# Optimization experiments

Measured on AMD Instinct MI355X. Metric: run time of the kernel, lower is better.

Reference implementation:

```python
import jax, jax.numpy as jnp
import numpy as np

B, S, D, H = 4, 1024, 1024, 16
DK = D // H
EPS = 1e-6

def setup_inputs() -> dict:
    key = jax.random.key(0)
    ks = jax.random.split(key, 7)
    scale = 1.0 / np.sqrt(D)
    return {
        "query": jax.random.normal(ks[0], (B, S, D), jnp.float32),
        "key": jax.random.normal(ks[1], (B, S, D), jnp.float32),
        "value": jax.random.normal(ks[2], (B, S, D), jnp.float32),
        "Wq": jax.random.normal(ks[3], (D, D), jnp.float32) * scale,
        "Wk": jax.random.normal(ks[4], (D, D), jnp.float32) * scale,
        "Wv": jax.random.normal(ks[5], (D, D), jnp.float32) * scale,
        "Wo": jax.random.normal(ks[6], (D, D), jnp.float32) * scale,
        "ln_gamma": jnp.ones((D,), jnp.float32),
        "ln_beta": jnp.zeros((D,), jnp.float32),
    }

def reference(query, key, value, Wq, Wk, Wv, Wo, ln_gamma, ln_beta):
    residual = query
    # projections (torch Linear: x @ W.T); reshape to [B,H,S,DK]
    def proj(x, W):
        y = jnp.einsum('bsd,ed->bse', x, W)
        return y.reshape(B, S, H, DK).transpose(0, 2, 1, 3)
    q, k, v = proj(query, Wq), proj(key, Wk), proj(value, Wv)
    scores = jnp.einsum('bhqd,bhkd->bhqk', q, k) / jnp.sqrt(jnp.float32(DK))
    p = jax.nn.softmax(scores, axis=-1)
    x = jnp.einsum('bhqk,bhkd->bhqd', p, v)
    x = x.transpose(0, 2, 1, 3).reshape(B, S, D)
    x = jnp.einsum('bsd,ed->bse', x, Wo)
    x = x + residual
    mu = jnp.mean(x, axis=-1, keepdims=True)
    var = jnp.var(x, axis=-1, keepdims=True)
    x = (x - mu) / jnp.sqrt(var + EPS) * ln_gamma + ln_beta
    return x
```

## Files before the change

kernel.cpp:

```cpp
#include <hip/hip_runtime.h>
#include <hip/hip_bf16.h>

#define B_ 4
#define S_ 1024
#define D_ 1024
#define H_ 16
#define DK_ 64
#define MROWS (B_*S_)

typedef short bf16x8 __attribute__((ext_vector_type(8)));
typedef float f32x4 __attribute__((ext_vector_type(4)));
typedef unsigned short u16;
typedef unsigned u32;
typedef u16 u16x4 __attribute__((ext_vector_type(4)));

__device__ __forceinline__ u16 f2bf(float f) {
    union { float f; unsigned u; } v; v.f = f;
    unsigned u = v.u;
    u += 0x7fff + ((u >> 16) & 1);
    return (u16)(u >> 16);
}

__device__ __forceinline__ void gld_lds16(const u16* gp, u16* lp) {
    __builtin_amdgcn_global_load_lds(
        (const __attribute__((address_space(1))) void*)gp,
        (__attribute__((address_space(3))) void*)lp,
        16, 0, 0);
}

__global__ __launch_bounds__(256) void pack_bf16(
    const float* __restrict__ q, const float* __restrict__ k, const float* __restrict__ v,
    const float* __restrict__ wq, const float* __restrict__ wk,
    const float* __restrict__ wv, const float* __restrict__ wo,
    u16* __restrict__ act_dst, u16* __restrict__ w_dst)
{
    const int NACT = 3 * MROWS * D_;
    const int NW   = 4 * D_ * D_;
    for (int c = blockIdx.x * blockDim.x + threadIdx.x;
         c < (NACT + NW) / 4; c += gridDim.x * blockDim.x) {
        int e = c * 4;
        const float* s; u16* d;
        if (e < NACT) {
            int t = e >> 22;
            int off = e & (4194304 - 1);
            s = (t == 0 ? q : t == 1 ? k : v) + off;
            d = act_dst + e;
        } else {
            int e2 = e - NACT;
            int t = e2 >> 20;
            int off = e2 & (1048576 - 1);
            s = (t == 0 ? wq : t == 1 ? wk : t == 2 ? wv : wo) + off;
            d = w_dst + e2;
        }
        float4 tv = *(const float4*)s;
        u16x4 o; o[0]=f2bf(tv.x); o[1]=f2bf(tv.y); o[2]=f2bf(tv.z); o[3]=f2bf(tv.w);
        *(u16x4*)d = o;
    }
}

template<int BM, bool EPI_RESID, bool VT>
__global__ __launch_bounds__(256) void gemm_fast(
    const u16* __restrict__ Ab, const u16* __restrict__ Wb,
    u16* __restrict__ Cb, float* __restrict__ Cf, const float* __restrict__ resid)
{
    constexpr int WN = (BM == 128) ? 2 : 4;
    constexpr int WCOLS = 128 / WN;
    constexpr int NR = WCOLS / 16;
    __shared__ u16 ldsA[BM * 64];
    __shared__ u16 ldsB[128 * 64];

    const int z = blockIdx.z;
    Ab += (size_t)z * MROWS * D_;
    Wb += (size_t)z * D_ * D_;
    if (!EPI_RESID) Cb += (size_t)z * MROWS * D_;

    const int tid = threadIdx.x, lane = tid & 63, wid = tid >> 6;
    const int wr = (BM == 128) ? (wid >> 1) : 0;
    const int wc = (BM == 128) ? (wid & 1) : wid;
    const int m0 = blockIdx.y * BM, n0 = blockIdx.x * 128;
    const int wbase = wid * 64;

    f32x4 acc[4][NR] = {};

    for (int kt = 0; kt < 1024; kt += 64) {
        __syncthreads();
        #pragma unroll
        for (int j = 0; j < BM / 32; ++j) {
            int ch = j * 256 + tid;
            int row = ch >> 3, c8 = (ch & 7) ^ (row & 7);
            gld_lds16(Ab + (size_t)(m0 + row) * 1024 + kt + c8 * 8,
                      &ldsA[(j * 256 + wbase) * 8]);
        }
        #pragma unroll
        for (int j = 0; j < 4; ++j) {
            int ch = j * 256 + tid;
            int row = ch >> 3, c8 = (ch & 7) ^ (row & 7);
            gld_lds16(Wb + (size_t)(n0 + row) * 1024 + kt + c8 * 8,
                      &ldsB[(j * 256 + wbase) * 8]);
        }
        __syncthreads();

        #pragma unroll
        for (int ks = 0; ks < 2; ++ks) {
            const int cb = ks * 32 + (lane >> 4) * 8;
            bf16x8 af[4], bfr[NR];
            #pragma unroll
            for (int m = 0; m < 4; ++m) {
                int row = wr * 64 + m * 16 + (lane & 15);
                af[m] = *(const bf16x8*)(&ldsA[row * 64 + (cb ^ ((row & 7) << 3))]);
            }
            #pragma unroll
            for (int n = 0; n < NR; ++n) {
                int row = wc * WCOLS + n * 16 + (lane & 15);
                bfr[n] = *(const bf16x8*)(&ldsB[row * 64 + (cb ^ ((row & 7) << 3))]);
            }
            #pragma unroll
            for (int m = 0; m < 4; ++m)
                #pragma unroll
                for (int n = 0; n < NR; ++n)
                    acc[m][n] = __builtin_amdgcn_mfma_f32_16x16x32_bf16(
                        af[m], bfr[n], acc[m][n], 0, 0, 0);
        }
    }

    if (VT && z == 2) {
        #pragma unroll
        for (int m = 0; m < 4; ++m)
            #pragma unroll
            for (int n = 0; n < NR; ++n) {
                u16x4 o;
                #pragma unroll
                for (int r = 0; r < 4; ++r) o[r] = f2bf(acc[m][n][r]);
                int grow = m0 + wr * 64 + m * 16 + (lane >> 4) * 4;
                int gcol = n0 + wc * WCOLS + n * 16 + (lane & 15);
                *(u16x4*)(&Cb[(size_t)gcol * MROWS + grow]) = o;
            }
    } else {
        #pragma unroll
        for (int m = 0; m < 4; ++m)
            #pragma unroll
            for (int n = 0; n < NR; ++n)
                #pragma unroll
                for (int r = 0; r < 4; ++r) {
                    int grow = m0 + wr * 64 + m * 16 + (lane >> 4) * 4 + r;
                    int gcol = n0 + wc * WCOLS + n * 16 + (lane & 15);
                    if (EPI_RESID)
                        Cf[(size_t)grow * 1024 + gcol] = acc[m][n][r] + resid[(size_t)grow * 1024 + gcol];
                    else
                        Cb[(size_t)grow * 1024 + gcol] = f2bf(acc[m][n][r]);
                }
    }
}

template<bool A_BF16, bool EPI_RESID>
__global__ __launch_bounds__(256) void gemm_bt(
    const void* __restrict__ Av, const float* __restrict__ Bw,
    u16* __restrict__ Cb, float* __restrict__ Cf,
    const float* __restrict__ resid, int M, int N, int K)
{
    __shared__ u16 lds[2][128 * 64];
    const int tid  = threadIdx.x;
    const int lane = tid & 63;
    const int wid  = tid >> 6;
    const int wr = wid >> 1, wc = wid & 1;
    const int m0 = blockIdx.y * 128, n0 = blockIdx.x * 128;

    f32x4 acc[4][4] = {};

    for (int kt = 0; kt < K; kt += 64) {
        #pragma unroll
        for (int j = 0; j < 8; ++j) {
            int idx4 = tid + 256 * j;
            int r = idx4 >> 4;
            int c = (idx4 & 15) * 4;
            u16x4 aw, bw;
            if (A_BF16) {
                const u16* Ab2 = (const u16*)Av;
                aw = *(const u16x4*)(Ab2 + (size_t)(m0 + r) * K + kt + c);
            } else {
                const float* Af = (const float*)Av;
                float4 t = *(const float4*)(Af + (size_t)(m0 + r) * K + kt + c);
                aw[0] = f2bf(t.x); aw[1] = f2bf(t.y); aw[2] = f2bf(t.z); aw[3] = f2bf(t.w);
            }
            {
                float4 t = *(const float4*)(Bw + (size_t)(n0 + r) * K + kt + c);
                bw[0] = f2bf(t.x); bw[1] = f2bf(t.y); bw[2] = f2bf(t.z); bw[3] = f2bf(t.w);
            }
            int sa = r * 64 + (c ^ ((r & 7) << 3));
            *(u16x4*)(&lds[0][sa]) = aw;
            *(u16x4*)(&lds[1][sa]) = bw;
        }
        __syncthreads();
        #pragma unroll
        for (int ks = 0; ks < 2; ++ks) {
            const int cb = ks * 32 + (lane >> 4) * 8;
            bf16x8 af[4], bfr[4];
            #pragma unroll
            for (int m = 0; m < 4; ++m) {
                int row = wr * 64 + m * 16 + (lane & 15);
                af[m] = *(const bf16x8*)(&lds[0][row * 64 + (cb ^ ((row & 7) << 3))]);
            }
            #pragma unroll
            for (int n = 0; n < 4; ++n) {
                int row = wc * 64 + n * 16 + (lane & 15);
                bfr[n] = *(const bf16x8*)(&lds[1][row * 64 + (cb ^ ((row & 7) << 3))]);
            }
            #pragma unroll
            for (int m = 0; m < 4; ++m)
                #pragma unroll
                for (int n = 0; n < 4; ++n)
                    acc[m][n] = __builtin_amdgcn_mfma_f32_16x16x32_bf16(
                        af[m], bfr[n], acc[m][n], 0, 0, 0);
        }
        __syncthreads();
    }

    #pragma unroll
    for (int m = 0; m < 4; ++m)
        #pragma unroll
        for (int n = 0; n < 4; ++n)
            #pragma unroll
            for (int r = 0; r < 4; ++r) {
                int grow = m0 + wr * 64 + m * 16 + (lane >> 4) * 4 + r;
                int gcol = n0 + wc * 64 + n * 16 + (lane & 15);
                float v = acc[m][n][r];
                if (EPI_RESID)
                    Cf[(size_t)grow * N + gcol] = v + resid[(size_t)grow * N + gcol];
                else
                    Cb[(size_t)grow * N + gcol] = f2bf(v);
            }
}

__global__ __launch_bounds__(256, 4) void attn_fwd3(
    const u16* __restrict__ Qg, const u16* __restrict__ Kg,
    const u16* __restrict__ Vt, u16* __restrict__ Og)
{
    __shared__ u16 qs[64 * 64];
    __shared__ u16 ks2[64 * 64];
    __shared__ u16 vsT[64 * 64];
    __shared__ u16 ps[64 * 64];

    const int tid = threadIdx.x, lane = tid & 63, w = tid >> 6;
    const int g = lane >> 4, ql = lane & 15;

    const int f2 = blockIdx.x;
    const int f = (f2 & 127) * 8 + (f2 >> 7);
    const int qt = f & 15, h = (f >> 4) & 15, b = f >> 8;
    const int q0 = qt * 64;
    const size_t rbase = (size_t)b * S_;
    const int cb0 = h * DK_;

    #pragma unroll
    for (int j = 0; j < 2; ++j) {
        int idx8 = tid + 256 * j;
        int r = idx8 >> 3, c = (idx8 & 7) * 8;
        bf16x8 t = *(const bf16x8*)(Qg + (rbase + q0 + r) * D_ + cb0 + c);
        *(bf16x8*)(&qs[r * 64 + (c ^ ((r & 7) << 3))]) = t;
    }
    __syncthreads();

    bf16x8 qb[2];
    {
        const int q = w * 16 + ql;
        #pragma unroll
        for (int ks = 0; ks < 2; ++ks) {
            int c = 32 * ks + 8 * g;
            qb[ks] = *(const bf16x8*)(&qs[q * 64 + (c ^ ((q & 7) << 3))]);
        }
    }

    float mrow = -1e30f, lrow = 0.f;
    f32x4 xacc[4] = {};

    for (int jt = 0; jt < 16; ++jt) {
        const int kv0 = jt * 64;
        __syncthreads();
        #pragma unroll
        for (int j = 0; j < 2; ++j) {
            int idx8 = tid + 256 * j;
            int r = idx8 >> 3, c = (idx8 & 7) * 8;
            bf16x8 t = *(const bf16x8*)(Kg + (rbase + kv0 + r) * D_ + cb0 + c);
            *(bf16x8*)(&ks2[r * 64 + (c ^ ((r & 7) << 3))]) = t;
            bf16x8 tv = *(const bf16x8*)(Vt + (size_t)(cb0 + r) * MROWS + rbase + kv0 + c);
            *(bf16x8*)(&vsT[r * 64 + (c ^ ((r & 7) << 3))]) = tv;
        }
        __syncthreads();

        f32x4 sacc[4] = {};
        __builtin_amdgcn_s_setprio(1);
        #pragma unroll
        for (int ks = 0; ks < 2; ++ks) {
            #pragma unroll
            for (int n = 0; n < 4; ++n) {
                int krow = n * 16 + ql;
                int c = 32 * ks + 8 * g;
                bf16x8 kf = *(const bf16x8*)(&ks2[krow * 64 + (c ^ ((krow & 7) << 3))]);
                sacc[n] = __builtin_amdgcn_mfma_f32_16x16x32_bf16(kf, qb[ks], sacc[n], 0, 0, 0);
            }
        }
        __builtin_amdgcn_s_setprio(0);

        float mt = sacc[0][0];
        #pragma unroll
        for (int n = 0; n < 4; ++n)
            #pragma unroll
            for (int r = 0; r < 4; ++r) mt = fmaxf(mt, sacc[n][r]);
        mt = fmaxf(mt, __shfl_xor(mt, 16));
        mt = fmaxf(mt, __shfl_xor(mt, 32));
        float mnew = fmaxf(mrow, mt * 0.125f);
        float alpha = __expf(mrow - mnew);
        float rsum = 0.f;
        u16 pb[16];
        #pragma unroll
        for (int n = 0; n < 4; ++n)
            #pragma unroll
            for (int r = 0; r < 4; ++r) {
                float p = __expf(sacc[n][r] * 0.125f - mnew);
                rsum += p;
                pb[n * 4 + r] = f2bf(p);
            }
        rsum += __shfl_xor(rsum, 16);
        rsum += __shfl_xor(rsum, 32);
        lrow = lrow * alpha + rsum;
        mrow = mnew;

        {
            const int q = w * 16 + ql;
            #pragma unroll
            for (int n = 0; n < 4; ++n) {
                int c = 16 * n + 4 * g;
                *(u16x4*)(&ps[q * 64 + (c ^ ((q & 7) << 3))]) = *(const u16x4*)(&pb[n * 4]);
            }
        }
        asm volatile("s_waitcnt lgkmcnt(0)" ::: "memory");
        __builtin_amdgcn_sched_barrier(0);

        bf16x8 pa[2];
        {
            const int q = w * 16 + ql;
            #pragma unroll
            for (int ks = 0; ks < 2; ++ks) {
                int c = 32 * ks + 8 * g;
                pa[ks] = *(const bf16x8*)(&ps[q * 64 + (c ^ ((q & 7) << 3))]);
            }
        }
        #pragma unroll
        for (int r = 0; r < 4; ++r) {
            float a_r = __shfl(alpha, 4 * g + r);
            #pragma unroll
            for (int n2 = 0; n2 < 4; ++n2) xacc[n2][r] *= a_r;
        }

        __builtin_amdgcn_s_setprio(1);
        #pragma unroll
        for (int ks = 0; ks < 2; ++ks)
            #pragma unroll
            for (int n2 = 0; n2 < 4; ++n2) {
                int vrow = n2 * 16 + ql;
                int c2 = 32 * ks + 8 * g;
                bf16x8 bv = *(const bf16x8*)(&vsT[vrow * 64 + (c2 ^ ((vrow & 7) << 3))]);
                xacc[n2] = __builtin_amdgcn_mfma_f32_16x16x32_bf16(pa[ks], bv, xacc[n2], 0, 0, 0);
            }
        __builtin_amdgcn_s_setprio(0);
    }

    float linv[4];
    #pragma unroll
    for (int r = 0; r < 4; ++r) linv[r] = 1.f / __shfl(lrow, 4 * g + r);
    #pragma unroll
    for (int n2 = 0; n2 < 4; ++n2)
        #pragma unroll
        for (int r = 0; r < 4; ++r) {
            int qrow = q0 + w * 16 + 4 * g + r;
            int col = cb0 + n2 * 16 + ql;
            Og[(rbase + qrow) * D_ + col] = f2bf(xacc[n2][r] * linv[r]);
        }
}

__global__ __launch_bounds__(256) void attn_fwd(
    const u16* __restrict__ Qg, const u16* __restrict__ Kg,
    const u16* __restrict__ Vg, u16* __restrict__ Og)
{
    __shared__ u16 qs[64 * 64], ks2[64 * 64], vt[64 * 64], ps[64 * 64];
    const int tid = threadIdx.x, lane = tid & 63, w = tid >> 6;
    const int b = blockIdx.z, h = blockIdx.y, q0 = blockIdx.x * 64;
    const size_t rbase = (size_t)b * S_;
    const int cb0 = h * DK_;

    #pragma unroll
    for (int j = 0; j < 4; ++j) {
        int idx4 = tid + 256 * j;
        int r = idx4 >> 4, c = (idx4 & 15) * 4;
        u16x4 t = *(const u16x4*)(Qg + (rbase + q0 + r) * D_ + cb0 + c);
        *(u16x4*)(&qs[r * 64 + (c ^ ((r & 7) << 3))]) = t;
    }

    float mrow[4], lrow[4];
    f32x4 xacc[4] = {};
    #pragma unroll
    for (int r = 0; r < 4; ++r) { mrow[r] = -1e30f; lrow[r] = 0.f; }

    for (int jt = 0; jt < 16; ++jt) {
        const int kv0 = jt * 64;
        __syncthreads();
        #pragma unroll
        for (int j = 0; j < 4; ++j) {
            int idx4 = tid + 256 * j;
            int r = idx4 >> 4, c = (idx4 & 15) * 4;
            u16x4 t = *(const u16x4*)(Kg + (rbase + kv0 + r) * D_ + cb0 + c);
            *(u16x4*)(&ks2[r * 64 + (c ^ ((r & 7) << 3))]) = t;
            u16x4 tv = *(const u16x4*)(Vg + (rbase + kv0 + r) * D_ + cb0 + c);
            #pragma unroll
            for (int jj = 0; jj < 4; ++jj) {
                int d = c + jj;
                vt[d * 64 + (r ^ ((d & 7) << 3))] = tv[jj];
            }
        }
        __syncthreads();

        f32x4 sacc[4] = {};
        #pragma unroll
        for (int ks = 0; ks < 2; ++ks) {
            const int cb = ks * 32 + (lane >> 4) * 8;
            int qrow = w * 16 + (lane & 15);
            bf16x8 aq = *(const bf16x8*)(&qs[qrow * 64 + (cb ^ ((qrow & 7) << 3))]);
            #pragma unroll
            for (int n = 0; n < 4; ++n) {
                int krow = n * 16 + (lane & 15);
                bf16x8 bk = *(const bf16x8*)(&ks2[krow * 64 + (cb ^ ((krow & 7) << 3))]);
                sacc[n] = __builtin_amdgcn_mfma_f32_16x16x32_bf16(aq, bk, sacc[n], 0, 0, 0);
            }
        }

        #pragma unroll
        for (int r = 0; r < 4; ++r) {
            float mx = fmaxf(fmaxf(sacc[0][r], sacc[1][r]),
                             fmaxf(sacc[2][r], sacc[3][r]));
            mx = fmaxf(mx, __shfl_xor(mx, 1));
            mx = fmaxf(mx, __shfl_xor(mx, 2));
            mx = fmaxf(mx, __shfl_xor(mx, 4));
            mx = fmaxf(mx, __shfl_xor(mx, 8));
            float mnew = fmaxf(mrow[r], mx * 0.125f);
            float alpha = __expf(mrow[r] - mnew);
            float p[4], rsum = 0.f;
            #pragma unroll
            for (int n = 0; n < 4; ++n) { p[n] = __expf(sacc[n][r] * 0.125f - mnew); rsum += p[n]; }
            rsum += __shfl_xor(rsum, 1);
            rsum += __shfl_xor(rsum, 2);
            rsum += __shfl_xor(rsum, 4);
            rsum += __shfl_xor(rsum, 8);
            lrow[r] = lrow[r] * alpha + rsum;
            mrow[r] = mnew;
            int qrow = w * 16 + (lane >> 4) * 4 + r;
            #pragma unroll
            for (int n = 0; n < 4; ++n) {
                xacc[n][r] *= alpha;
                int col = n * 16 + (lane & 15);
                ps[qrow * 64 + (col ^ ((qrow & 7) << 3))] = f2bf(p[n]);
            }
        }
        __syncthreads();

        #pragma unroll
        for (int ks = 0; ks < 2; ++ks) {
            const int cb = ks * 32 + (lane >> 4) * 8;
            int prow = w * 16 + (lane & 15);
            bf16x8 ap = *(const bf16x8*)(&ps[prow * 64 + (cb ^ ((prow & 7) << 3))]);
            #pragma unroll
            for (int n = 0; n < 4; ++n) {
                int vrow = n * 16 + (lane & 15);
                bf16x8 bv = *(const bf16x8*)(&vt[vrow * 64 + (cb ^ ((vrow & 7) << 3))]);
                xacc[n] = __builtin_amdgcn_mfma_f32_16x16x32_bf16(ap, bv, xacc[n], 0, 0, 0);
            }
        }
    }

    #pragma unroll
    for (int n = 0; n < 4; ++n)
        #pragma unroll
        for (int r = 0; r < 4; ++r) {
            int qrow = q0 + w * 16 + (lane >> 4) * 4 + r;
            int col = cb0 + n * 16 + (lane & 15);
            Og[(rbase + qrow) * D_ + col] = f2bf(xacc[n][r] / lrow[r]);
        }
}

__global__ __launch_bounds__(256) void ln_inplace(
    float* __restrict__ Y, const float* __restrict__ g, const float* __restrict__ bt)
{
    __shared__ float red[2][4];
    const int row = blockIdx.x, tid = threadIdx.x;
    float4 v = *(const float4*)(Y + (size_t)row * D_ + tid * 4);
    float s = v.x + v.y + v.z + v.w;
    float q = v.x * v.x + v.y * v.y + v.z * v.z + v.w * v.w;
    #pragma unroll
    for (int m = 1; m < 64; m <<= 1) { s += __shfl_xor(s, m); q += __shfl_xor(q, m); }
    const int w = tid >> 6, lane = tid & 63;
    if (lane == 0) { red[0][w] = s; red[1][w] = q; }
    __syncthreads();
    s = red[0][0] + red[0][1] + red[0][2] + red[0][3];
    q = red[1][0] + red[1][1] + red[1][2] + red[1][3];
    float mu = s * (1.f / 1024.f);
    float var = q * (1.f / 1024.f) - mu * mu;
    float rstd = rsqrtf(var + 1e-6f);
    float4 gv = *(const float4*)(g + tid * 4);
    float4 bv = *(const float4*)(bt + tid * 4);
    v.x = (v.x - mu) * rstd * gv.x + bv.x;
    v.y = (v.y - mu) * rstd * gv.y + bv.y;
    v.z = (v.z - mu) * rstd * gv.z + bv.z;
    v.w = (v.w - mu) * rstd * gv.w + bv.w;
    *(float4*)(Y + (size_t)row * D_ + tid * 4) = v;
}

extern "C" void kernel_launch(void* const* d_in, const int* in_sizes, int n_in,
                              void* d_out, int out_size, void* d_ws, size_t ws_size,
                              hipStream_t stream)
{
    const float* query = (const float*)d_in[0];
    const float* key   = (const float*)d_in[1];
    const float* value = (const float*)d_in[2];
    const float* Wq    = (const float*)d_in[3];
    const float* Wk    = (const float*)d_in[4];
    const float* Wv    = (const float*)d_in[5];
    const float* Wo    = (const float*)d_in[6];
    const float* gamma = (const float*)d_in[7];
    const float* beta  = (const float*)d_in[8];
    float* out = (float*)d_out;

    const size_t ACT = (size_t)MROWS * D_;
    const size_t WSZ = (size_t)D_ * D_;
    const size_t NEED = (3 * ACT + 4 * WSZ + 3 * ACT) * 2;

    if (ws_size >= NEED) {
        u16* actb = (u16*)d_ws;
        u16* wb   = actb + 3 * ACT;
        u16* pb   = wb + 4 * WSZ;
        u16* Ap   = actb;

        pack_bf16<<<2048, 256, 0, stream>>>(query, key, value, Wq, Wk, Wv, Wo, actb, wb);
        gemm_fast<128, false, true><<<dim3(8, 32, 3), 256, 0, stream>>>(actb, wb, pb, nullptr, nullptr);
        attn_fwd3<<<1024, 256, 0, stream>>>(pb, pb + ACT, pb + 2 * ACT, Ap);
        gemm_fast<64, true, false><<<dim3(8, 64, 1), 256, 0, stream>>>(Ap, wb + 3 * WSZ, nullptr, out, query);
        ln_inplace<<<MROWS, 256, 0, stream>>>(out, gamma, beta);
    } else {
        u16* Qp = (u16*)d_ws;
        u16* Kp = Qp + ACT;
        u16* Vp = Kp + ACT;
        u16* Ap = Vp + ACT;
        dim3 gg(D_ / 128, MROWS / 128);
        gemm_bt<false, false><<<gg, 256, 0, stream>>>(query, Wq, Qp, nullptr, nullptr, MROWS, D_, D_);
        gemm_bt<false, false><<<gg, 256, 0, stream>>>(key,   Wk, Kp, nullptr, nullptr, MROWS, D_, D_);
        gemm_bt<false, false><<<gg, 256, 0, stream>>>(value, Wv, Vp, nullptr, nullptr, MROWS, D_, D_);
        attn_fwd<<<dim3(S_ / 64, H_, B_), 256, 0, stream>>>(Qp, Kp, Vp, Ap);
        gemm_bt<true, true><<<gg, 256, 0, stream>>>(Ap, Wo, nullptr, out, query, MROWS, D_, D_);
        ln_inplace<<<MROWS, 256, 0, stream>>>(out, gamma, beta);
    }
}
```

Baseline: 127.1 us.

## Double-buffer LDS tiles in GEMM and attention with async global-to-LDS prefetch

```diff
diff --git a/kernel.cpp b/kernel.cpp
--- a/kernel.cpp
+++ b/kernel.cpp
@@ -27,6 +27,12 @@
         (__attribute__((address_space(3))) void*)lp,
         16, 0, 0);
 }
+
+#define VMCNT0_BARRIER() do { \
+    asm volatile("s_waitcnt vmcnt(0)" ::: "memory"); \
+    __builtin_amdgcn_s_barrier(); \
+    asm volatile("" ::: "memory"); \
+} while (0)
 
 __global__ __launch_bounds__(256) void pack_bf16(
     const float* __restrict__ q, const float* __restrict__ k, const float* __restrict__ v,
@@ -66,8 +72,8 @@
     constexpr int WN = (BM == 128) ? 2 : 4;
     constexpr int WCOLS = 128 / WN;
     constexpr int NR = WCOLS / 16;
-    __shared__ u16 ldsA[BM * 64];
-    __shared__ u16 ldsB[128 * 64];
+    __shared__ u16 ldsA[2][BM * 64];
+    __shared__ u16 ldsB[2][128 * 64];
 
     const int z = blockIdx.z;
     Ab += (size_t)z * MROWS * D_;
@@ -80,25 +86,31 @@
     const int m0 = blockIdx.y * BM, n0 = blockIdx.x * 128;
     const int wbase = wid * 64;
 
-    f32x4 acc[4][NR] = {};
-
-    for (int kt = 0; kt < 1024; kt += 64) {
-        __syncthreads();
+    auto stage = [&](int p, int kt) {
         #pragma unroll
         for (int j = 0; j < BM / 32; ++j) {
             int ch = j * 256 + tid;
             int row = ch >> 3, c8 = (ch & 7) ^ (row & 7);
             gld_lds16(Ab + (size_t)(m0 + row) * 1024 + kt + c8 * 8,
-                      &ldsA[(j * 256 + wbase) * 8]);
+                      &ldsA[p][(j * 256 + wbase) * 8]);
         }
         #pragma unroll
         for (int j = 0; j < 4; ++j) {
             int ch = j * 256 + tid;
             int row = ch >> 3, c8 = (ch & 7) ^ (row & 7);
             gld_lds16(Wb + (size_t)(n0 + row) * 1024 + kt + c8 * 8,
-                      &ldsB[(j * 256 + wbase) * 8]);
-        }
-        __syncthreads();
+                      &ldsB[p][(j * 256 + wbase) * 8]);
+        }
+    };
+
+    f32x4 acc[4][NR] = {};
+
+    stage(0, 0);
+    VMCNT0_BARRIER();
+
+    for (int it = 0; it < 16; ++it) {
+        const int cur = it & 1;
+        if (it < 15) stage(cur ^ 1, (it + 1) * 64);
 
         #pragma unroll
         for (int ks = 0; ks < 2; ++ks) {
@@ -107,12 +119,12 @@
             #pragma unroll
             for (int m = 0; m < 4; ++m) {
                 int row = wr * 64 + m * 16 + (lane & 15);
-                af[m] = *(const bf16x8*)(&ldsA[row * 64 + (cb ^ ((row & 7) << 3))]);
+                af[m] = *(const bf16x8*)(&ldsA[cur][row * 64 + (cb ^ ((row & 7) << 3))]);
             }
             #pragma unroll
             for (int n = 0; n < NR; ++n) {
                 int row = wc * WCOLS + n * 16 + (lane & 15);
-                bfr[n] = *(const bf16x8*)(&ldsB[row * 64 + (cb ^ ((row & 7) << 3))]);
+                bfr[n] = *(const bf16x8*)(&ldsB[cur][row * 64 + (cb ^ ((row & 7) << 3))]);
             }
             #pragma unroll
             for (int m = 0; m < 4; ++m)
@@ -121,6 +133,8 @@
                     acc[m][n] = __builtin_amdgcn_mfma_f32_16x16x32_bf16(
                         af[m], bfr[n], acc[m][n], 0, 0, 0);
         }
+
+        if (it < 15) VMCNT0_BARRIER();
     }
 
     if (VT && z == 2) {
@@ -231,13 +245,13 @@
             }
 }
 
-__global__ __launch_bounds__(256, 4) void attn_fwd3(
+__global__ __launch_bounds__(256, 4) void attn_fwd4(
     const u16* __restrict__ Qg, const u16* __restrict__ Kg,
     const u16* __restrict__ Vt, u16* __restrict__ Og)
 {
     __shared__ u16 qs[64 * 64];
-    __shared__ u16 ks2[64 * 64];
-    __shared__ u16 vsT[64 * 64];
+    __shared__ u16 ks2[2][64 * 64];
+    __shared__ u16 vsT[2][64 * 64];
     __shared__ u16 ps[64 * 64];
 
     const int tid = threadIdx.x, lane = tid & 63, w = tid >> 6;
@@ -249,15 +263,34 @@
     const int q0 = qt * 64;
     const size_t rbase = (size_t)b * S_;
     const int cb0 = h * DK_;
+    const int wbase = w * 64;
+
+    auto stage_kv = [&](int p, int kv0) {
+        #pragma unroll
+        for (int j = 0; j < 2; ++j) {
+            int ch = j * 256 + tid;
+            int row = ch >> 3, c8 = (ch & 7) ^ (row & 7);
+            gld_lds16(Kg + (rbase + kv0 + row) * D_ + cb0 + c8 * 8,
+                      &ks2[p][(j * 256 + wbase) * 8]);
+        }
+        #pragma unroll
+        for (int j = 0; j < 2; ++j) {
+            int ch = j * 256 + tid;
+            int row = ch >> 3, c8 = (ch & 7) ^ (row & 7);
+            gld_lds16(Vt + (size_t)(cb0 + row) * MROWS + rbase + kv0 + c8 * 8,
+                      &vsT[p][(j * 256 + wbase) * 8]);
+        }
+    };
 
     #pragma unroll
     for (int j = 0; j < 2; ++j) {
-        int idx8 = tid + 256 * j;
-        int r = idx8 >> 3, c = (idx8 & 7) * 8;
-        bf16x8 t = *(const bf16x8*)(Qg + (rbase + q0 + r) * D_ + cb0 + c);
-        *(bf16x8*)(&qs[r * 64 + (c ^ ((r & 7) << 3))]) = t;
-    }
-    __syncthreads();
+        int ch = j * 256 + tid;
+        int row = ch >> 3, c8 = (ch & 7) ^ (row & 7);
+        gld_lds16(Qg + (rbase + q0 + row) * D_ + cb0 + c8 * 8,
+                  &qs[(j * 256 + wbase) * 8]);
+    }
+    stage_kv(0, 0);
+    VMCNT0_BARRIER();
 
     bf16x8 qb[2];
     {
@@ -273,18 +306,8 @@
     f32x4 xacc[4] = {};
 
     for (int jt = 0; jt < 16; ++jt) {
-        const int kv0 = jt * 64;
-        __syncthreads();
-        #pragma unroll
-        for (int j = 0; j < 2; ++j) {
-            int idx8 = tid + 256 * j;
-            int r = idx8 >> 3, c = (idx8 & 7) * 8;
-            bf16x8 t = *(const bf16x8*)(Kg + (rbase + kv0 + r) * D_ + cb0 + c);
-            *(bf16x8*)(&ks2[r * 64 + (c ^ ((r & 7) << 3))]) = t;
-            bf16x8 tv = *(const bf16x8*)(Vt + (size_t)(cb0 + r) * MROWS + rbase + kv0 + c);
-            *(bf16x8*)(&vsT[r * 64 + (c ^ ((r & 7) << 3))]) = tv;
-        }
-        __syncthreads();
+        const int cur = jt & 1;
+        if (jt < 15) stage_kv(cur ^ 1, (jt + 1) * 64);
 
         f32x4 sacc[4] = {};
         __builtin_amdgcn_s_setprio(1);
@@ -294,7 +317,7 @@
             for (int n = 0; n < 4; ++n) {
                 int krow = n * 16 + ql;
                 int c = 32 * ks + 8 * g;
-                bf16x8 kf = *(const bf16x8*)(&ks2[krow * 64 + (c ^ ((krow & 7) << 3))]);
+                bf16x8 kf = *(const bf16x8*)(&ks2[cur][krow * 64 + (c ^ ((krow & 7) << 3))]);
                 sacc[n] = __builtin_amdgcn_mfma_f32_16x16x32_bf16(kf, qb[ks], sacc[n], 0, 0, 0);
             }
         }
@@ -358,10 +381,12 @@
             for (int n2 = 0; n2 < 4; ++n2) {
                 int vrow = n2 * 16 + ql;
                 int c2 = 32 * ks + 8 * g;
-                bf16x8 bv = *(const bf16x8*)(&vsT[vrow * 64 + (c2 ^ ((vrow & 7) << 3))]);
+                bf16x8 bv = *(const bf16x8*)(&vsT[cur][vrow * 64 + (c2 ^ ((vrow & 7) << 3))]);
                 xacc[n2] = __builtin_amdgcn_mfma_f32_16x16x32_bf16(pa[ks], bv, xacc[n2], 0, 0, 0);
             }
         __builtin_amdgcn_s_setprio(0);
+
+        if (jt < 15) VMCNT0_BARRIER();
     }
 
     float linv[4];
@@ -539,7 +564,7 @@
 
         pack_bf16<<<2048, 256, 0, stream>>>(query, key, value, Wq, Wk, Wv, Wo, actb, wb);
         gemm_fast<128, false, true><<<dim3(8, 32, 3), 256, 0, stream>>>(actb, wb, pb, nullptr, nullptr);
-        attn_fwd3<<<1024, 256, 0, stream>>>(pb, pb + ACT, pb + 2 * ACT, Ap);
+        attn_fwd4<<<1024, 256, 0, stream>>>(pb, pb + ACT, pb + 2 * ACT, Ap);
         gemm_fast<64, true, false><<<dim3(8, 64, 1), 256, 0, stream>>>(Ap, wb + 3 * WSZ, nullptr, out, query);
         ln_inplace<<<MROWS, 256, 0, stream>>>(out, gamma, beta);
     } else {
```

Measured after the change: 144.3 us. 13.5% more time.

## Widen attention blocks to 128 queries with LDS-direct K/V staging and remap GEMM tiles

Applied to the files above, without the earlier changes.

```diff
diff --git a/kernel.cpp b/kernel.cpp
--- a/kernel.cpp
+++ b/kernel.cpp
@@ -69,15 +69,24 @@
     __shared__ u16 ldsA[BM * 64];
     __shared__ u16 ldsB[128 * 64];
 
-    const int z = blockIdx.z;
+    const int gx = gridDim.x, gy = gridDim.y, gz = gridDim.z;
+    const int nwg = gx * gy * gz;
+    const int flat = blockIdx.x + gx * (blockIdx.y + gy * blockIdx.z);
+    const int f = (flat & 7) * (nwg >> 3) + (flat >> 3);
+    const int bx = f % gx;
+    const int rem = f / gx;
+    const int by = rem % gy;
+    const int z = rem / gy;
+
     Ab += (size_t)z * MROWS * D_;
     Wb += (size_t)z * D_ * D_;
-    if (!EPI_RESID) Cb += (size_t)z * MROWS * D_;
+    const u16* CbT = Cb + (EPI_RESID ? 0 : (size_t)z * MROWS * D_);
+    u16* Cbz = (u16*)CbT;
 
     const int tid = threadIdx.x, lane = tid & 63, wid = tid >> 6;
     const int wr = (BM == 128) ? (wid >> 1) : 0;
     const int wc = (BM == 128) ? (wid & 1) : wid;
-    const int m0 = blockIdx.y * BM, n0 = blockIdx.x * 128;
+    const int m0 = by * BM, n0 = bx * 128;
     const int wbase = wid * 64;
 
     f32x4 acc[4][NR] = {};
@@ -133,7 +142,7 @@
                 for (int r = 0; r < 4; ++r) o[r] = f2bf(acc[m][n][r]);
                 int grow = m0 + wr * 64 + m * 16 + (lane >> 4) * 4;
                 int gcol = n0 + wc * WCOLS + n * 16 + (lane & 15);
-                *(u16x4*)(&Cb[(size_t)gcol * MROWS + grow]) = o;
+                *(u16x4*)(&Cbz[(size_t)gcol * MROWS + grow]) = o;
             }
     } else {
         #pragma unroll
@@ -147,7 +156,7 @@
                     if (EPI_RESID)
                         Cf[(size_t)grow * 1024 + gcol] = acc[m][n][r] + resid[(size_t)grow * 1024 + gcol];
                     else
-                        Cb[(size_t)grow * 1024 + gcol] = f2bf(acc[m][n][r]);
+                        Cbz[(size_t)grow * 1024 + gcol] = f2bf(acc[m][n][r]);
                 }
     }
 }
@@ -231,32 +240,46 @@
             }
 }
 
-__global__ __launch_bounds__(256, 4) void attn_fwd3(
+__global__ __launch_bounds__(512, 4) void attn_fwd5(
     const u16* __restrict__ Qg, const u16* __restrict__ Kg,
     const u16* __restrict__ Vt, u16* __restrict__ Og)
 {
-    __shared__ u16 qs[64 * 64];
+    __shared__ u16 qs[128 * 64];
     __shared__ u16 ks2[64 * 64];
     __shared__ u16 vsT[64 * 64];
-    __shared__ u16 ps[64 * 64];
+    __shared__ u16 ps[128 * 64];
 
     const int tid = threadIdx.x, lane = tid & 63, w = tid >> 6;
     const int g = lane >> 4, ql = lane & 15;
 
-    const int f2 = blockIdx.x;
-    const int f = (f2 & 127) * 8 + (f2 >> 7);
-    const int qt = f & 15, h = (f >> 4) & 15, b = f >> 8;
-    const int q0 = qt * 64;
+    const int bid = blockIdx.x;
+    const int f = (bid & 7) * 64 + (bid >> 3);
+    const int qt = f & 7, h = (f >> 3) & 15, b = f >> 7;
+    const int q0 = qt * 128;
     const size_t rbase = (size_t)b * S_;
     const int cb0 = h * DK_;
 
+    auto stage_kv = [&](int kv0) {
+        {
+            int ch = tid;
+            int row = ch >> 3, c8 = (ch & 7) ^ (row & 7);
+            gld_lds16(Kg + (rbase + kv0 + row) * D_ + cb0 + c8 * 8, &ks2[w * 512]);
+        }
+        {
+            int ch = tid;
+            int row = ch >> 3, c8 = (ch & 7) ^ (row & 7);
+            gld_lds16(Vt + (size_t)(cb0 + row) * MROWS + rbase + kv0 + c8 * 8, &vsT[w * 512]);
+        }
+    };
+
     #pragma unroll
     for (int j = 0; j < 2; ++j) {
-        int idx8 = tid + 256 * j;
-        int r = idx8 >> 3, c = (idx8 & 7) * 8;
-        bf16x8 t = *(const bf16x8*)(Qg + (rbase + q0 + r) * D_ + cb0 + c);
-        *(bf16x8*)(&qs[r * 64 + (c ^ ((r & 7) << 3))]) = t;
-    }
+        int idx = j * 512 + tid;
+        int row = idx >> 3, c8 = (idx & 7) ^ (row & 7);
+        gld_lds16(Qg + (rbase + q0 + row) * D_ + cb0 + c8 * 8,
+                  &qs[(j * 512 + w * 64) * 8]);
+    }
+    stage_kv(0);
     __syncthreads();
 
     bf16x8 qb[2];
@@ -273,19 +296,6 @@
     f32x4 xacc[4] = {};
 
     for (int jt = 0; jt < 16; ++jt) {
-        const int kv0 = jt * 64;
-        __syncthreads();
-        #pragma unroll
-        for (int j = 0; j < 2; ++j) {
-            int idx8 = tid + 256 * j;
-            int r = idx8 >> 3, c = (idx8 & 7) * 8;
-            bf16x8 t = *(const bf16x8*)(Kg + (rbase + kv0 + r) * D_ + cb0 + c);
-            *(bf16x8*)(&ks2[r * 64 + (c ^ ((r & 7) << 3))]) = t;
-            bf16x8 tv = *(const bf16x8*)(Vt + (size_t)(cb0 + r) * MROWS + rbase + kv0 + c);
-            *(bf16x8*)(&vsT[r * 64 + (c ^ ((r & 7) << 3))]) = tv;
-        }
-        __syncthreads();
-
         f32x4 sacc[4] = {};
         __builtin_amdgcn_s_setprio(1);
         #pragma unroll
@@ -362,6 +372,12 @@
                 xacc[n2] = __builtin_amdgcn_mfma_f32_16x16x32_bf16(pa[ks], bv, xacc[n2], 0, 0, 0);
             }
         __builtin_amdgcn_s_setprio(0);
+
+        if (jt < 15) {
+            __syncthreads();
+            stage_kv((jt + 1) * 64);
+            __syncthreads();
+        }
     }
 
     float linv[4];
@@ -539,7 +555,7 @@
 
         pack_bf16<<<2048, 256, 0, stream>>>(query, key, value, Wq, Wk, Wv, Wo, actb, wb);
         gemm_fast<128, false, true><<<dim3(8, 32, 3), 256, 0, stream>>>(actb, wb, pb, nullptr, nullptr);
-        attn_fwd3<<<1024, 256, 0, stream>>>(pb, pb + ACT, pb + 2 * ACT, Ap);
+        attn_fwd5<<<512, 512, 0, stream>>>(pb, pb + ACT, pb + 2 * ACT, Ap);
         gemm_fast<64, true, false><<<dim3(8, 64, 1), 256, 0, stream>>>(Ap, wb + 3 * WSZ, nullptr, out, query);
         ln_inplace<<<MROWS, 256, 0, stream>>>(out, gamma, beta);
     } else {
```

Measured after the change: 122.5 us. 1.04x faster.
